# Performance work log

Measured on AMD Instinct MI355X. Metric: run time of the kernel, lower is better.

## Reference

```python
import jax, jax.numpy as jnp
import numpy as np

N_NODES = 100000
N_EDGES = 1600000
IN_CH = 256
HID_CH = 256
OUT_CH = 40


def gcn_conv(x, W, b, src, dst, n):
    """PyG GCNConv with default symmetric normalization and self-loops,
    edge_weight = 1. out_i = sum_{j->i} d_i^{-1/2} d_j^{-1/2} (x_j W) + d_i^{-1} (x_i W) + b
    where d includes the self-loop (+1)."""
    h = x @ W  # [n, out]
    deg = jnp.zeros((n,), x.dtype).at[dst].add(1.0) + 1.0  # +1 self-loop
    dinv = jax.lax.rsqrt(deg)
    norm = dinv[src] * dinv[dst]                      # [E]
    msg = h[src] * norm[:, None]                      # [E, out] gather
    agg = jnp.zeros_like(h).at[dst].add(msg)          # scatter-add
    agg = agg + h * (dinv * dinv)[:, None]            # self-loop term
    return agg + b


def setup_inputs() -> dict:
    key = jax.random.key(0)
    ks = jax.random.split(key, 8)
    x = jax.random.normal(ks[0], (N_NODES, IN_CH), jnp.float32)
    edge_index = jax.random.randint(ks[1], (2, N_EDGES), 0, N_NODES, jnp.int64)
    s1 = 1.0 / np.sqrt(IN_CH)
    s2 = 1.0 / np.sqrt(HID_CH)
    W1 = jax.random.normal(ks[2], (IN_CH, HID_CH), jnp.float32) * s1
    b1 = jnp.zeros((HID_CH,), jnp.float32)
    W2 = jax.random.normal(ks[3], (HID_CH, HID_CH), jnp.float32) * s2
    b2 = jnp.zeros((HID_CH,), jnp.float32)
    W3 = jax.random.normal(ks[4], (HID_CH, OUT_CH), jnp.float32) * s2
    b3 = jnp.zeros((OUT_CH,), jnp.float32)
    return {"x": x, "edge_index": edge_index, "W1": W1, "b1": b1,
            "W2": W2, "b2": b2, "W3": W3, "b3": b3}


def reference(x, edge_index, W1, b1, W2, b2, W3, b3):
    src, dst = edge_index[0], edge_index[1]
    n = x.shape[0]
    # layer 1: conv -> relu (batch_norm=False, dropout inactive in eval)
    h = jax.nn.relu(gcn_conv(x, W1, b1, src, dst, n))
    # layer 2
    h = jax.nn.relu(gcn_conv(h, W2, b2, src, dst, n))
    # final layer + log_softmax
    h = gcn_conv(h, W3, b3, src, dst, n)
    return jax.nn.log_softmax(h, axis=-1)
```

## Files before the change

### kernel.cpp

```cpp
#include <hip/hip_runtime.h>
#include <math.h>
#include <cstddef>

#define NN 100000
#define NE 1600000
#define CH 256
#define OC 40

typedef __attribute__((ext_vector_type(8))) short bf16x8;
typedef __attribute__((ext_vector_type(4))) float f32x4;

static __device__ __forceinline__ unsigned short f2bf(float f) {
    unsigned int u = __float_as_uint(f);
    unsigned int r = (u + 0x7FFFu + ((u >> 16) & 1u)) >> 16;
    return (unsigned short)r;
}
static __device__ __forceinline__ float bflo(unsigned int u) {
    return __uint_as_float(u << 16);
}
static __device__ __forceinline__ float bfhi(unsigned int u) {
    return __uint_as_float(u & 0xFFFF0000u);
}
static __device__ __forceinline__ uint4 ld_f32x8_to_bf8(const float* p) {
    float4 a = *reinterpret_cast<const float4*>(p);
    float4 b = *reinterpret_cast<const float4*>(p + 4);
    uint4 r;
    r.x = f2bf(a.x) | ((unsigned)f2bf(a.y) << 16);
    r.y = f2bf(a.z) | ((unsigned)f2bf(a.w) << 16);
    r.z = f2bf(b.x) | ((unsigned)f2bf(b.y) << 16);
    r.w = f2bf(b.z) | ((unsigned)f2bf(b.w) << 16);
    return r;
}


__global__ void hist_kernel(const int* __restrict__ dst, int* __restrict__ deg, int E) {
    int i = blockIdx.x * blockDim.x + threadIdx.x;
    int st = gridDim.x * blockDim.x;
    for (; i < E; i += st) atomicAdd(&deg[dst[i]], 1);
}

__global__ void dinv_kernel(const int* __restrict__ deg, float* __restrict__ dinv, int n) {
    int i = blockIdx.x * blockDim.x + threadIdx.x;
    if (i < n) dinv[i] = rsqrtf((float)deg[i] + 1.0f);
}

__global__ __launch_bounds__(256) void scan1_kernel(const int* __restrict__ deg,
        int* __restrict__ row_ptr, int* __restrict__ bsum, int n) {
    __shared__ int s[256];
    int t = threadIdx.x;
    int i = blockIdx.x * 256 + t;
    int v = (i < n) ? deg[i] + 1 : 0;
    s[t] = v;
    __syncthreads();
    #pragma unroll
    for (int off = 1; off < 256; off <<= 1) {
        int u = (t >= off) ? s[t - off] : 0;
        __syncthreads();
        s[t] += u;
        __syncthreads();
    }
    if (i < n) row_ptr[i] = s[t] - v;
    if (t == 255) bsum[blockIdx.x] = s[255];
}

__global__ __launch_bounds__(512) void scan2_kernel(const int* __restrict__ bsum,
        int* __restrict__ boff, int* __restrict__ row_ptr, int nb, int n) {
    __shared__ int s[512];
    int t = threadIdx.x;
    int v = (t < nb) ? bsum[t] : 0;
    s[t] = v;
    __syncthreads();
    #pragma unroll
    for (int off = 1; off < 512; off <<= 1) {
        int u = (t >= off) ? s[t - off] : 0;
        __syncthreads();
        s[t] += u;
        __syncthreads();
    }
    if (t < nb) boff[t] = s[t] - v;
    if (t == nb - 1) row_ptr[n] = s[t];
}

__global__ __launch_bounds__(256) void scan3_kernel(int* __restrict__ row_ptr,
        const int* __restrict__ boff, int n) {
    int i = blockIdx.x * 256 + threadIdx.x;
    if (i < n) row_ptr[i] += boff[i >> 8];
}

__global__ __launch_bounds__(256) void cpy_kernel(const int* __restrict__ rp,
        int* __restrict__ cursor, int n) {
    int i = blockIdx.x * 256 + threadIdx.x;
    if (i < n) cursor[i] = rp[i];
}

__global__ void fill_kernel(const int* __restrict__ src, const int* __restrict__ dst,
                            const int* __restrict__ row_ptr, int* __restrict__ cursor,
                            int* __restrict__ csr_src, int E, int n) {
    int i = blockIdx.x * blockDim.x + threadIdx.x;
    int st = gridDim.x * blockDim.x;
    int total = E + n;
    for (; i < total; i += st) {
        if (i < E) {
            int s = src[i], d = dst[i];
            int pos = atomicAdd(&cursor[d], 1);
            csr_src[pos] = s;
        } else {
            int v = i - E;
            csr_src[row_ptr[v + 1] - 1] = v;
        }
    }
}


__global__ void wtrans_kernel(const float* __restrict__ W, unsigned short* __restrict__ Wt) {
    __shared__ float tile[16][17];
    int k = blockIdx.y * 16 + threadIdx.y;
    int n = blockIdx.x * 16 + threadIdx.x;
    tile[threadIdx.y][threadIdx.x] = W[(size_t)k * 256 + n];
    __syncthreads();
    int on = blockIdx.x * 16 + threadIdx.y;
    int ok = blockIdx.y * 16 + threadIdx.x;
    Wt[(size_t)on * 256 + ok] = f2bf(tile[threadIdx.x][threadIdx.y]);
}

__global__ __launch_bounds__(256) void gemm_l1_kernel(
        const float* __restrict__ A, const unsigned short* __restrict__ Wt,
        unsigned short* __restrict__ C, int M) {
    __shared__ __align__(16) unsigned short As[128 * 40];
    __shared__ __align__(16) unsigned short Bs[128 * 40];
    const int t = threadIdx.x;
    const int l = t & 63;
    const int w = t >> 6;
    const int wr = w >> 1, wc = w & 1;
    const int row0 = blockIdx.x * 128;
    const int col0 = blockIdx.y * 128;

    f32x4 acc[4][4];
    #pragma unroll
    for (int m = 0; m < 4; m++)
        #pragma unroll
        for (int n = 0; n < 4; n++) acc[m][n] = (f32x4){0.f, 0.f, 0.f, 0.f};

    const int sr = t >> 2;
    const int sc = (t & 3) * 8;
    const int rl = l & 15;
    const int kb = (l >> 4) * 8;

    uint4 va[2], ub[2];
    #pragma unroll
    for (int p = 0; p < 2; p++) {
        int r = sr + p * 64;
        int gr = row0 + r;
        va[p] = (gr < M) ? ld_f32x8_to_bf8(A + (size_t)gr * 256 + sc)
                         : make_uint4(0u, 0u, 0u, 0u);
        ub[p] = *reinterpret_cast<const uint4*>(Wt + (size_t)(col0 + r) * 256 + sc);
    }

    for (int k0 = 0; k0 < 256; k0 += 32) {
        #pragma unroll
        for (int p = 0; p < 2; p++) {
            int r = sr + p * 64;
            *reinterpret_cast<uint4*>(&As[r * 40 + sc]) = va[p];
            *reinterpret_cast<uint4*>(&Bs[r * 40 + sc]) = ub[p];
        }
        __syncthreads();
        if (k0 + 32 < 256) {
            #pragma unroll
            for (int p = 0; p < 2; p++) {
                int r = sr + p * 64;
                int gr = row0 + r;
                va[p] = (gr < M) ? ld_f32x8_to_bf8(A + (size_t)gr * 256 + k0 + 32 + sc)
                                 : make_uint4(0u, 0u, 0u, 0u);
                ub[p] = *reinterpret_cast<const uint4*>(Wt + (size_t)(col0 + r) * 256 + k0 + 32 + sc);
            }
        }
        bf16x8 af[4], bfr[4];
        #pragma unroll
        for (int m = 0; m < 4; m++)
            af[m] = *reinterpret_cast<const bf16x8*>(&As[(wr * 64 + m * 16 + rl) * 40 + kb]);
        #pragma unroll
        for (int n = 0; n < 4; n++)
            bfr[n] = *reinterpret_cast<const bf16x8*>(&Bs[(wc * 64 + n * 16 + rl) * 40 + kb]);
        #pragma unroll
        for (int m = 0; m < 4; m++)
            #pragma unroll
            for (int n = 0; n < 4; n++)
                acc[m][n] = __builtin_amdgcn_mfma_f32_16x16x32_bf16(af[m], bfr[n], acc[m][n], 0, 0, 0);
        __syncthreads();
    }
    const int rh = l >> 4;
    #pragma unroll
    for (int m = 0; m < 4; m++) {
        #pragma unroll
        for (int n = 0; n < 4; n++) {
            #pragma unroll
            for (int j = 0; j < 4; j++) {
                int gr = row0 + wr * 64 + m * 16 + rh * 4 + j;
                int gc = col0 + wc * 64 + n * 16 + rl;
                if (gr < M) C[(size_t)gr * 256 + gc] = f2bf(acc[m][n][j]);
            }
        }
    }
}

__global__ __launch_bounds__(256) void gemm_bf16_kernel(
        const unsigned short* __restrict__ A, const unsigned short* __restrict__ Wt,
        unsigned short* __restrict__ C, int M) {
    __shared__ __align__(16) unsigned short As[128 * 40];
    __shared__ __align__(16) unsigned short Bs[128 * 40];
    const int t = threadIdx.x;
    const int l = t & 63;
    const int w = t >> 6;
    const int wr = w >> 1, wc = w & 1;
    const int row0 = blockIdx.x * 128;
    const int col0 = blockIdx.y * 128;

    f32x4 acc[4][4];
    #pragma unroll
    for (int m = 0; m < 4; m++)
        #pragma unroll
        for (int n = 0; n < 4; n++) acc[m][n] = (f32x4){0.f, 0.f, 0.f, 0.f};

    const int sr = t >> 2;
    const int sc = (t & 3) * 8;
    const int rl = l & 15;
    const int kb = (l >> 4) * 8;

    uint4 va[2], ub[2];
    #pragma unroll
    for (int p = 0; p < 2; p++) {
        int r = sr + p * 64;
        int gr = row0 + r;
        va[p] = (gr < M) ? *reinterpret_cast<const uint4*>(A + (size_t)gr * 256 + sc)
                         : make_uint4(0u, 0u, 0u, 0u);
        ub[p] = *reinterpret_cast<const uint4*>(Wt + (size_t)(col0 + r) * 256 + sc);
    }

    for (int k0 = 0; k0 < 256; k0 += 32) {
        #pragma unroll
        for (int p = 0; p < 2; p++) {
            int r = sr + p * 64;
            *reinterpret_cast<uint4*>(&As[r * 40 + sc]) = va[p];
            *reinterpret_cast<uint4*>(&Bs[r * 40 + sc]) = ub[p];
        }
        __syncthreads();
        if (k0 + 32 < 256) {
            #pragma unroll
            for (int p = 0; p < 2; p++) {
                int r = sr + p * 64;
                int gr = row0 + r;
                va[p] = (gr < M) ? *reinterpret_cast<const uint4*>(A + (size_t)gr * 256 + k0 + 32 + sc)
                                 : make_uint4(0u, 0u, 0u, 0u);
                ub[p] = *reinterpret_cast<const uint4*>(Wt + (size_t)(col0 + r) * 256 + k0 + 32 + sc);
            }
        }
        bf16x8 af[4], bfr[4];
        #pragma unroll
        for (int m = 0; m < 4; m++)
            af[m] = *reinterpret_cast<const bf16x8*>(&As[(wr * 64 + m * 16 + rl) * 40 + kb]);
        #pragma unroll
        for (int n = 0; n < 4; n++)
            bfr[n] = *reinterpret_cast<const bf16x8*>(&Bs[(wc * 64 + n * 16 + rl) * 40 + kb]);
        #pragma unroll
        for (int m = 0; m < 4; m++)
            #pragma unroll
            for (int n = 0; n < 4; n++)
                acc[m][n] = __builtin_amdgcn_mfma_f32_16x16x32_bf16(af[m], bfr[n], acc[m][n], 0, 0, 0);
        __syncthreads();
    }
    const int rh = l >> 4;
    #pragma unroll
    for (int m = 0; m < 4; m++) {
        #pragma unroll
        for (int n = 0; n < 4; n++) {
            #pragma unroll
            for (int j = 0; j < 4; j++) {
                int gr = row0 + wr * 64 + m * 16 + rh * 4 + j;
                int gc = col0 + wc * 64 + n * 16 + rl;
                if (gr < M) C[(size_t)gr * 256 + gc] = f2bf(acc[m][n][j]);
            }
        }
    }
}

__global__ __launch_bounds__(256) void gemm40_kernel(const unsigned short* __restrict__ A,
                                                     const float* __restrict__ W,
                                                     float* __restrict__ C, int M) {
    __shared__ float Hs[128][65];
    __shared__ float Ws[64][40];
    const int t = threadIdx.x;
    const int tr = t & 127;
    const int tg = t >> 7;
    const int row0 = blockIdx.x * 128;
    float acc[20];
    #pragma unroll
    for (int j = 0; j < 20; j++) acc[j] = 0.f;

    const int hr = t >> 4;
    const int hc = (t & 15) << 2;

    for (int k0 = 0; k0 < 256; k0 += 64) {
        #pragma unroll
        for (int p = 0; p < 8; p++) {
            int r = hr + p * 16;
            int gr = row0 + r;
            uint2 u = make_uint2(0u, 0u);
            if (gr < M) u = *reinterpret_cast<const uint2*>(A + (size_t)gr * 256 + k0 + hc);
            Hs[r][hc] = bflo(u.x); Hs[r][hc + 1] = bfhi(u.x);
            Hs[r][hc + 2] = bflo(u.y); Hs[r][hc + 3] = bfhi(u.y);
        }
        for (int i = t; i < 64 * 40; i += 256) {
            int r = i / 40, c = i - r * 40;
            Ws[r][c] = W[(size_t)(k0 + r) * 40 + c];
        }
        __syncthreads();
        #pragma unroll 4
        for (int kk = 0; kk < 64; ++kk) {
            float a = Hs[tr][kk];
            float b[20];
            #pragma unroll
            for (int q = 0; q < 5; q++)
                *reinterpret_cast<float4*>(&b[q * 4]) =
                    *reinterpret_cast<float4*>(&Ws[kk][tg * 20 + q * 4]);
            #pragma unroll
            for (int j = 0; j < 20; j++) acc[j] = fmaf(a, b[j], acc[j]);
        }
        __syncthreads();
    }
    int gr = row0 + tr;
    if (gr < M) {
        #pragma unroll
        for (int q = 0; q < 5; q++) {
            float4 v = make_float4(acc[q * 4], acc[q * 4 + 1], acc[q * 4 + 2], acc[q * 4 + 3]);
            *reinterpret_cast<float4*>(C + (size_t)gr * 40 + tg * 20 + q * 4) = v;
        }
    }
}

__global__ __launch_bounds__(256) void aggb_kernel(const unsigned short* __restrict__ T,
        const int* __restrict__ row_ptr, const int* __restrict__ csr_src,
        const float* __restrict__ dinv, const float* __restrict__ bias,
        unsigned short* __restrict__ H, int n, int do_relu) {
    int wid = threadIdx.x >> 6, lane = threadIdx.x & 63;
    int node = blockIdx.x * 4 + wid;
    if (node >= n) return;
    int e0 = row_ptr[node], end = row_ptr[node + 1];
    float dn = dinv[node];
    float a0 = 0.f, a1 = 0.f, a2 = 0.f, a3 = 0.f;
    for (int base = e0; base < end; base += 64) {
        int cnt = min(64, end - base);
        int sv = 0; float wv = 0.f;
        if (lane < cnt) { sv = csr_src[base + lane]; wv = dinv[sv]; }
        int j = 0;
        for (; j + 3 < cnt; j += 4) {
            int s0 = __shfl(sv, j),     s1 = __shfl(sv, j + 1);
            int s2 = __shfl(sv, j + 2), s3 = __shfl(sv, j + 3);
            float w0 = __shfl(wv, j),     w1 = __shfl(wv, j + 1);
            float w2 = __shfl(wv, j + 2), w3 = __shfl(wv, j + 3);
            uint2 u0 = *reinterpret_cast<const uint2*>(T + (size_t)s0 * 256 + lane * 4);
            uint2 u1 = *reinterpret_cast<const uint2*>(T + (size_t)s1 * 256 + lane * 4);
            uint2 u2 = *reinterpret_cast<const uint2*>(T + (size_t)s2 * 256 + lane * 4);
            uint2 u3 = *reinterpret_cast<const uint2*>(T + (size_t)s3 * 256 + lane * 4);
            a0 = fmaf(w0, bflo(u0.x), a0); a1 = fmaf(w0, bfhi(u0.x), a1);
            a2 = fmaf(w0, bflo(u0.y), a2); a3 = fmaf(w0, bfhi(u0.y), a3);
            a0 = fmaf(w1, bflo(u1.x), a0); a1 = fmaf(w1, bfhi(u1.x), a1);
            a2 = fmaf(w1, bflo(u1.y), a2); a3 = fmaf(w1, bfhi(u1.y), a3);
            a0 = fmaf(w2, bflo(u2.x), a0); a1 = fmaf(w2, bfhi(u2.x), a1);
            a2 = fmaf(w2, bflo(u2.y), a2); a3 = fmaf(w2, bfhi(u2.y), a3);
            a0 = fmaf(w3, bflo(u3.x), a0); a1 = fmaf(w3, bfhi(u3.x), a1);
            a2 = fmaf(w3, bflo(u3.y), a2); a3 = fmaf(w3, bfhi(u3.y), a3);
        }
        for (; j < cnt; ++j) {
            int s0 = __shfl(sv, j);
            float w0 = __shfl(wv, j);
            uint2 u0 = *reinterpret_cast<const uint2*>(T + (size_t)s0 * 256 + lane * 4);
            a0 = fmaf(w0, bflo(u0.x), a0); a1 = fmaf(w0, bfhi(u0.x), a1);
            a2 = fmaf(w0, bflo(u0.y), a2); a3 = fmaf(w0, bfhi(u0.y), a3);
        }
    }
    float4 bb = reinterpret_cast<const float4*>(bias)[lane];
    a0 = fmaf(a0, dn, bb.x); a1 = fmaf(a1, dn, bb.y);
    a2 = fmaf(a2, dn, bb.z); a3 = fmaf(a3, dn, bb.w);
    if (do_relu) {
        a0 = fmaxf(a0, 0.f); a1 = fmaxf(a1, 0.f);
        a2 = fmaxf(a2, 0.f); a3 = fmaxf(a3, 0.f);
    }
    uint2 o;
    o.x = f2bf(a0) | ((unsigned)f2bf(a1) << 16);
    o.y = f2bf(a2) | ((unsigned)f2bf(a3) << 16);
    *reinterpret_cast<uint2*>(H + (size_t)node * 256 + lane * 4) = o;
}

__global__ __launch_bounds__(256) void agg40_kernel(const float* __restrict__ T3,
        const int* __restrict__ row_ptr, const int* __restrict__ csr_src,
        const float* __restrict__ dinv, const float* __restrict__ bias,
        float* __restrict__ Out, int n) {
    int wid = threadIdx.x >> 6, lane = threadIdx.x & 63;
    int node = blockIdx.x * 4 + wid;
    if (node >= n) return;
    bool act = lane < OC;
    int e0 = row_ptr[node], end = row_ptr[node + 1];
    float dn = dinv[node];
    float acc = 0.f;
    for (int base = e0; base < end; base += 64) {
        int cnt = min(64, end - base);
        int sv = 0; float wv = 0.f;
        if (lane < cnt) { sv = csr_src[base + lane]; wv = dinv[sv]; }
        int j = 0;
        for (; j + 3 < cnt; j += 4) {
            int s0 = __shfl(sv, j),     s1 = __shfl(sv, j + 1);
            int s2 = __shfl(sv, j + 2), s3 = __shfl(sv, j + 3);
            float w0 = __shfl(wv, j),     w1 = __shfl(wv, j + 1);
            float w2 = __shfl(wv, j + 2), w3 = __shfl(wv, j + 3);
            float v0 = act ? T3[(size_t)s0 * OC + lane] : 0.f;
            float v1 = act ? T3[(size_t)s1 * OC + lane] : 0.f;
            float v2 = act ? T3[(size_t)s2 * OC + lane] : 0.f;
            float v3 = act ? T3[(size_t)s3 * OC + lane] : 0.f;
            acc = fmaf(w0, v0, acc);
            acc = fmaf(w1, v1, acc);
            acc = fmaf(w2, v2, acc);
            acc = fmaf(w3, v3, acc);
        }
        for (; j < cnt; ++j) {
            int s0 = __shfl(sv, j);
            float w0 = __shfl(wv, j);
            float v0 = act ? T3[(size_t)s0 * OC + lane] : 0.f;
            acc = fmaf(w0, v0, acc);
        }
    }
    float bb = act ? bias[lane] : 0.f;
    float x = act ? (acc * dn + bb) : -INFINITY;
    float m = x;
    #pragma unroll
    for (int off = 32; off; off >>= 1) m = fmaxf(m, __shfl_xor(m, off));
    float ex = act ? expf(x - m) : 0.f;
    float ssum = ex;
    #pragma unroll
    for (int off = 32; off; off >>= 1) ssum += __shfl_xor(ssum, off);
    if (act) Out[(size_t)node * OC + lane] = x - m - logf(ssum);
}


extern "C" void kernel_launch(void* const* d_in, const int* in_sizes, int n_in,
                              void* d_out, int out_size, void* d_ws, size_t ws_size,
                              hipStream_t stream) {
    const float* x  = (const float*)d_in[0];
    const int* ei   = (const int*)d_in[1];
    const int* esrc = ei;
    const int* edst = ei + NE;
    const float* W1 = (const float*)d_in[2];
    const float* b1 = (const float*)d_in[3];
    const float* W2 = (const float*)d_in[4];
    const float* b2 = (const float*)d_in[5];
    const float* W3 = (const float*)d_in[6];
    const float* b3 = (const float*)d_in[7];
    float* out = (float*)d_out;

    char* p = (char*)d_ws;
    int* deg      = (int*)p;   p += 400000;
    int* cursor   = (int*)p;   p += 400000;
    int* row_ptr  = (int*)p;   p += 400128;
    float* dinv   = (float*)p; p += 400000;
    int* bsum     = (int*)p;   p += 2048;
    int* boff     = (int*)p;   p += 2048;
    int* csr_src  = (int*)p;   p += (size_t)(NE + NN) * 4;
    unsigned short* Wt1 = (unsigned short*)p; p += 256 * 256 * 2;
    unsigned short* Wt2 = (unsigned short*)p; p += 256 * 256 * 2;
    unsigned short* Tb  = (unsigned short*)p; p += (size_t)NN * CH * 2;
    unsigned short* Hb  = (unsigned short*)p; p += (size_t)NN * CH * 2;
    float* T3     = (float*)p; p += (size_t)NN * OC * 4;

    hipMemsetAsync(deg, 0, 400000, stream);

    const int nb = (NN + 255) / 256;

    hist_kernel<<<2048, 256, 0, stream>>>(edst, deg, NE);
    dinv_kernel<<<nb, 256, 0, stream>>>(deg, dinv, NN);
    scan1_kernel<<<nb, 256, 0, stream>>>(deg, row_ptr, bsum, NN);
    scan2_kernel<<<1, 512, 0, stream>>>(bsum, boff, row_ptr, nb, NN);
    scan3_kernel<<<nb, 256, 0, stream>>>(row_ptr, boff, NN);
    cpy_kernel<<<nb, 256, 0, stream>>>(row_ptr, cursor, NN);
    fill_kernel<<<2048, 256, 0, stream>>>(esrc, edst, row_ptr, cursor, csr_src, NE, NN);

    {
        dim3 g(16, 16), b(16, 16);
        wtrans_kernel<<<g, b, 0, stream>>>(W1, Wt1);
        wtrans_kernel<<<g, b, 0, stream>>>(W2, Wt2);
    }

    dim3 gg((NN + 127) / 128, 2);
    gemm_l1_kernel<<<gg, 256, 0, stream>>>(x, Wt1, Tb, NN);
    aggb_kernel<<<NN / 4, 256, 0, stream>>>(Tb, row_ptr, csr_src, dinv, b1, Hb, NN, 1);
    gemm_bf16_kernel<<<gg, 256, 0, stream>>>(Hb, Wt2, Tb, NN);
    aggb_kernel<<<NN / 4, 256, 0, stream>>>(Tb, row_ptr, csr_src, dinv, b2, Hb, NN, 1);
    gemm40_kernel<<<(NN + 127) / 128, 256, 0, stream>>>(Hb, W3, T3, NN);
    agg40_kernel<<<NN / 4, 256, 0, stream>>>(T3, row_ptr, csr_src, dinv, b3, out, NN);
}
```

Before: 864.0 us.

## Replace atomic CSR build with two-pass bucketed partition using LDS

Replaces the global-atomic degree histogram and scatter-based CSR fill with a bucket partition. Edges are first binned into 128 destination-range buckets through a staging buffer, then each bucket block counts degrees and builds its CSR segment with LDS atomics before writing it out coalesced. This targets the cost of random global atomics and scattered writes into the CSR arrays. In exchange it adds extra kernel launches, a 12.8 MB staging pass, and per-bucket work with only 128 blocks, which may leave much of the GPU idle.

```diff
diff --git a/kernel.cpp b/kernel.cpp
--- a/kernel.cpp
+++ b/kernel.cpp
@@ -6,6 +6,11 @@
 #define NE 1600000
 #define CH 256
 #define OC 40
+
+#define NBKT 128
+#define BKN  782
+#define ACH  4096
+#define CAPB 14848
 
 typedef __attribute__((ext_vector_type(8))) short bf16x8;
 typedef __attribute__((ext_vector_type(4))) float f32x4;
@@ -33,10 +38,104 @@
 }
 
 
-__global__ void hist_kernel(const int* __restrict__ dst, int* __restrict__ deg, int E) {
-    int i = blockIdx.x * blockDim.x + threadIdx.x;
-    int st = gridDim.x * blockDim.x;
-    for (; i < E; i += st) atomicAdd(&deg[dst[i]], 1);
+__global__ __launch_bounds__(256) void bhist_kernel(const int* __restrict__ dst,
+        int* __restrict__ gh, int E) {
+    __shared__ int h[NBKT];
+    int t = threadIdx.x;
+    if (t < NBKT) h[t] = 0;
+    __syncthreads();
+    int i0 = blockIdx.x * ACH;
+    for (int i = i0 + t; i < i0 + ACH && i < E; i += 256)
+        atomicAdd(&h[(unsigned)dst[i] / BKN], 1);
+    __syncthreads();
+    if (t < NBKT && h[t]) atomicAdd(&gh[t], h[t]);
+}
+
+__global__ __launch_bounds__(128) void bscan_kernel(const int* __restrict__ gh,
+        int* __restrict__ bbase, int* __restrict__ gcur) {
+    __shared__ int s[NBKT];
+    int t = threadIdx.x;
+    int v = gh[t];
+    s[t] = v;
+    __syncthreads();
+    #pragma unroll
+    for (int off = 1; off < NBKT; off <<= 1) {
+        int u = (t >= off) ? s[t - off] : 0;
+        __syncthreads();
+        s[t] += u;
+        __syncthreads();
+    }
+    int e = s[t] - v;
+    bbase[t] = e;
+    gcur[t] = e;
+}
+
+__global__ __launch_bounds__(256) void passA_kernel(const int* __restrict__ src,
+        const int* __restrict__ dst, int* __restrict__ gcur,
+        int2* __restrict__ stag, int E) {
+    __shared__ int2 pairs[ACH];
+    __shared__ unsigned char pbkt[ACH];
+    __shared__ int h[NBKT], lofs[NBKT], gofs[NBKT];
+    int t = threadIdx.x;
+    if (t < NBKT) h[t] = 0;
+    __syncthreads();
+
+    int i0 = blockIdx.x * ACH;
+    int cnt = min(ACH, E - i0);
+
+    int myb[ACH / 256], myr[ACH / 256], mys[ACH / 256], myd[ACH / 256];
+    int k = 0;
+    for (int i = t; i < cnt; i += 256, ++k) {
+        int s = src[i0 + i], d = dst[i0 + i];
+        int b = (unsigned)d / BKN;
+        mys[k] = s; myd[k] = d; myb[k] = b;
+        myr[k] = atomicAdd(&h[b], 1);
+    }
+    __syncthreads();
+    {
+        __shared__ int sc[NBKT];
+        if (t < NBKT) sc[t] = h[t];
+        __syncthreads();
+        #pragma unroll
+        for (int off = 1; off < NBKT; off <<= 1) {
+            int u = (t >= off && t < NBKT) ? sc[t - off] : 0;
+            __syncthreads();
+            if (t < NBKT) sc[t] += u;
+            __syncthreads();
+        }
+        if (t < NBKT) lofs[t] = sc[t] - h[t];
+    }
+    __syncthreads();
+    k = 0;
+    for (int i = t; i < cnt; i += 256, ++k) {
+        int p = lofs[myb[k]] + myr[k];
+        pairs[p] = make_int2(mys[k], myd[k]);
+        pbkt[p] = (unsigned char)myb[k];
+    }
+    if (t < NBKT && h[t]) gofs[t] = atomicAdd(&gcur[t], h[t]);
+    __syncthreads();
+    for (int j = t; j < cnt; j += 256) {
+        int b = pbkt[j];
+        stag[gofs[b] + (j - lofs[b])] = pairs[j];
+    }
+}
+
+__global__ __launch_bounds__(256) void passB1_kernel(const int2* __restrict__ stag,
+        const int* __restrict__ bbase, const int* __restrict__ gh,
+        int* __restrict__ deg, int n) {
+    __shared__ int lh[BKN];
+    int b = blockIdx.x;
+    int t = threadIdx.x;
+    int node0 = b * BKN;
+    int nn = min(BKN, n - node0);
+    if (nn <= 0) return;
+    for (int i = t; i < nn; i += 256) lh[i] = 0;
+    __syncthreads();
+    int e0 = bbase[b], cnt = gh[b];
+    for (int i = t; i < cnt; i += 256)
+        atomicAdd(&lh[stag[e0 + i].y - node0], 1);
+    __syncthreads();
+    for (int i = t; i < nn; i += 256) deg[node0 + i] = lh[i];
 }
 
 __global__ void dinv_kernel(const int* __restrict__ deg, float* __restrict__ dinv, int n) {
@@ -87,28 +186,36 @@
     if (i < n) row_ptr[i] += boff[i >> 8];
 }
 
-__global__ __launch_bounds__(256) void cpy_kernel(const int* __restrict__ rp,
-        int* __restrict__ cursor, int n) {
-    int i = blockIdx.x * 256 + threadIdx.x;
-    if (i < n) cursor[i] = rp[i];
-}
-
-__global__ void fill_kernel(const int* __restrict__ src, const int* __restrict__ dst,
-                            const int* __restrict__ row_ptr, int* __restrict__ cursor,
-                            int* __restrict__ csr_src, int E, int n) {
-    int i = blockIdx.x * blockDim.x + threadIdx.x;
-    int st = gridDim.x * blockDim.x;
-    int total = E + n;
-    for (; i < total; i += st) {
-        if (i < E) {
-            int s = src[i], d = dst[i];
-            int pos = atomicAdd(&cursor[d], 1);
-            csr_src[pos] = s;
-        } else {
-            int v = i - E;
-            csr_src[row_ptr[v + 1] - 1] = v;
-        }
-    }
+__global__ __launch_bounds__(256) void passB2_kernel(const int2* __restrict__ stag,
+        const int* __restrict__ bbase, const int* __restrict__ gh,
+        const int* __restrict__ row_ptr, int* __restrict__ csr_src, int n) {
+    __shared__ int lds_out[CAPB];
+    __shared__ int lds_cur[BKN];
+    int b = blockIdx.x;
+    int t = threadIdx.x;
+    int node0 = b * BKN;
+    int nn = min(BKN, n - node0);
+    if (nn <= 0) return;
+    int base = row_ptr[node0];
+    int span = row_ptr[node0 + nn] - base;
+    for (int i = t; i < nn; i += 256) lds_cur[i] = row_ptr[node0 + i] - base;
+    __syncthreads();
+    int e0 = bbase[b], cnt = gh[b];
+    for (int i = t; i < cnt; i += 256) {
+        int2 pr = stag[e0 + i];
+        int p = atomicAdd(&lds_cur[pr.y - node0], 1);
+        if (p < CAPB) lds_out[p] = pr.x;
+        else csr_src[base + p] = pr.x;
+    }
+    for (int i = t; i < nn; i += 256) {
+        int v = node0 + i;
+        int p = row_ptr[v + 1] - 1 - base;
+        if (p < CAPB) lds_out[p] = v;
+        else csr_src[base + p] = v;
+    }
+    __syncthreads();
+    int lim = min(span, CAPB);
+    for (int j = t; j < lim; j += 256) csr_src[base + j] = lds_out[j];
 }
 
 
@@ -458,11 +565,14 @@
 
     char* p = (char*)d_ws;
     int* deg      = (int*)p;   p += 400000;
-    int* cursor   = (int*)p;   p += 400000;
     int* row_ptr  = (int*)p;   p += 400128;
     float* dinv   = (float*)p; p += 400000;
+    int* gh       = (int*)p;   p += 512;
+    int* bbase    = (int*)p;   p += 512;
+    int* gcur     = (int*)p;   p += 512;
     int* bsum     = (int*)p;   p += 2048;
     int* boff     = (int*)p;   p += 2048;
+    int2* stag    = (int2*)p;  p += (size_t)NE * 8;
     int* csr_src  = (int*)p;   p += (size_t)(NE + NN) * 4;
     unsigned short* Wt1 = (unsigned short*)p; p += 256 * 256 * 2;
     unsigned short* Wt2 = (unsigned short*)p; p += 256 * 256 * 2;
@@ -470,17 +580,20 @@
     unsigned short* Hb  = (unsigned short*)p; p += (size_t)NN * CH * 2;
     float* T3     = (float*)p; p += (size_t)NN * OC * 4;
 
-    hipMemsetAsync(deg, 0, 400000, stream);
+    hipMemsetAsync(gh, 0, 512, stream);
 
     const int nb = (NN + 255) / 256;
-
-    hist_kernel<<<2048, 256, 0, stream>>>(edst, deg, NE);
+    const int nba = (NE + ACH - 1) / ACH;
+
+    bhist_kernel<<<nba, 256, 0, stream>>>(edst, gh, NE);
+    bscan_kernel<<<1, NBKT, 0, stream>>>(gh, bbase, gcur);
+    passA_kernel<<<nba, 256, 0, stream>>>(esrc, edst, gcur, stag, NE);
+    passB1_kernel<<<NBKT, 256, 0, stream>>>(stag, bbase, gh, deg, NN);
     dinv_kernel<<<nb, 256, 0, stream>>>(deg, dinv, NN);
     scan1_kernel<<<nb, 256, 0, stream>>>(deg, row_ptr, bsum, NN);
     scan2_kernel<<<1, 512, 0, stream>>>(bsum, boff, row_ptr, nb, NN);
     scan3_kernel<<<nb, 256, 0, stream>>>(row_ptr, boff, NN);
-    cpy_kernel<<<nb, 256, 0, stream>>>(row_ptr, cursor, NN);
-    fill_kernel<<<2048, 256, 0, stream>>>(esrc, edst, row_ptr, cursor, csr_src, NE, NN);
+    passB2_kernel<<<NBKT, 256, 0, stream>>>(stag, bbase, gh, row_ptr, csr_src, NN);
 
     {
         dim3 g(16, 16), b(16, 16);
```

Result: faster. 741.1 us (-14.2%).
